# Kernel tuning notes

Measured on AMD Instinct MI355X. Metric: run time of the kernel, lower is better.

Reference implementation:

```python
import jax, jax.numpy as jnp
import numpy as np

B, N, M, H, W = 8, 8192, 4096, 128, 128


def setup_inputs() -> dict:
    key = jax.random.key(0)
    k1, k2, k3, k4 = jax.random.split(key, 4)
    xc_off_grid = jax.random.uniform(k1, (B, N, 2), dtype=jnp.float32)
    yc_off_grid = jax.random.normal(k2, (B, N), dtype=jnp.float32)
    # regular grid coords: meshgrid of two sorted 1-D axes, stacked on last dim
    xs = jnp.linspace(0.0, 1.0, H, dtype=jnp.float32)
    ys = jnp.linspace(0.0, 1.0, W, dtype=jnp.float32)
    gx, gy = jnp.meshgrid(xs, ys, indexing='ij')  # [H,W]
    xc_on_grid = jnp.broadcast_to(jnp.stack([gx, gy], -1), (B, H, W, 2))
    yc_on_grid = jax.random.normal(k3, (B, H, W), dtype=jnp.float32)
    # targets slightly outside [0,1] so interpn fill_value path is exercised
    xt = jax.random.uniform(k4, (B, M, 2), minval=-0.05, maxval=1.05, dtype=jnp.float32)
    mix_prop_logit = jnp.asarray(0.0, dtype=jnp.float32)
    return {"xc_off_grid": xc_off_grid, "yc_off_grid": yc_off_grid,
            "xc_on_grid": xc_on_grid, "yc_on_grid": yc_on_grid,
            "xt": xt, "mix_prop_logit": mix_prop_logit}


def _bilinear(xs, ys, vals, pts, fill):
    # interpn((xs, ys), vals, pts, bounds_error=False, fill_value=fill)
    x, y = pts[:, 0], pts[:, 1]
    ix = jnp.clip(jnp.searchsorted(xs, x, side='right') - 1, 0, xs.shape[0] - 2)
    iy = jnp.clip(jnp.searchsorted(ys, y, side='right') - 1, 0, ys.shape[0] - 2)
    wx = (x - xs[ix]) / (xs[ix + 1] - xs[ix])
    wy = (y - ys[iy]) / (ys[iy + 1] - ys[iy])
    v00 = vals[ix, iy]
    v01 = vals[ix, iy + 1]
    v10 = vals[ix + 1, iy]
    v11 = vals[ix + 1, iy + 1]
    v = ((1 - wx) * (1 - wy) * v00 + (1 - wx) * wy * v01
         + wx * (1 - wy) * v10 + wx * wy * v11)
    oob = (x < xs[0]) | (x > xs[-1]) | (y < ys[0]) | (y > ys[-1])
    return jnp.where(oob, fill, v)


def _per_batch(xc_off, yc_off, xc_on, yc_on, pts):
    # scattered interpolation: nearest-neighbor gather (stands in for
    # scipy griddata's Delaunay-linear; same irregular-access pattern)
    d2 = jnp.sum((pts[:, None, :] - xc_off[None, :, :]) ** 2, axis=-1)  # [M,N]
    yt_off = yc_off[jnp.argmin(d2, axis=1)]  # [M]
    # regular-grid bilinear, fill with grid mean outside bounds
    yt_on = _bilinear(xc_on[:, 0, 0], xc_on[0, :, 1], yc_on, pts, yc_on.mean())
    return yt_off, yt_on


def reference(xc_off_grid, yc_off_grid, xc_on_grid, yc_on_grid, xt, mix_prop_logit):
    yt_off, yt_on = jax.vmap(_per_batch)(xc_off_grid, yc_off_grid,
                                         xc_on_grid, yc_on_grid, xt)
    mix = jax.nn.sigmoid(mix_prop_logit)
    return mix * yt_off + (1 - mix) * yt_on  # [B, M]
```

## Files before the change

### kernel.cpp

```cpp
#include <hip/hip_runtime.h>
#include <math.h>
#include <float.h>

#define BB 8
#define NN 8192
#define MM 4096
#define HH 128
#define WW 128

#define G    32
#define GG   (G * G)
#define CELL (1.0f / G)

#define WS_COUNTS_OFF 256
#define WS_STARTS_OFF 33024
#define WS_CELLS_OFF  65824
#define WS_NEEDED     (WS_CELLS_OFF + (size_t)BB * NN * 16)

__device__ __forceinline__ int clampi(int v, int lo, int hi) {
    return v < lo ? lo : (v > hi ? hi : v);
}

__global__ __launch_bounds__(256)
void count_kernel(const float* __restrict__ xc_off,
                  int* __restrict__ counts) {
    const int idx = blockIdx.x * blockDim.x + threadIdx.x;
    const int b = idx >> 13;
    const float2 c = ((const float2*)xc_off)[idx];
    const int gx = clampi((int)(c.x * (float)G), 0, G - 1);
    const int gy = clampi((int)(c.y * (float)G), 0, G - 1);
    atomicAdd(&counts[b * GG + gx * G + gy], 1);
}

__global__ __launch_bounds__(1024)
void scan_mean_kernel(int* __restrict__ counts,
                      int* __restrict__ starts,
                      const float* __restrict__ yc_on,
                      float* __restrict__ means) {
    const int b = blockIdx.x, tid = threadIdx.x;
    __shared__ int   wsum[16];
    __shared__ float partial[4];

    const int orig = counts[b * GG + tid];
    int x = orig;
    const int lane = tid & 63, wid = tid >> 6;
    for (int off = 1; off < 64; off <<= 1) {
        int y = __shfl_up(x, off, 64);
        if (lane >= off) x += y;
    }
    if (lane == 63) wsum[wid] = x;
    __syncthreads();
    if (tid < 16) {
        int w = wsum[tid];
        for (int off = 1; off < 16; off <<= 1) {
            int y = __shfl_up(w, off, 16);
            if (tid >= off) w += y;
        }
        wsum[tid] = w;
    }
    __syncthreads();
    const int incl = x + (wid ? wsum[wid - 1] : 0);
    const int excl = incl - orig;
    starts[b * (GG + 1) + tid] = excl;
    if (tid == GG - 1) starts[b * (GG + 1) + GG] = incl;
    counts[b * GG + tid] = excl;

    float s = 0.f;
    if (tid < 256) {
        const float* p = yc_on + b * (HH * WW);
        for (int i = tid; i < HH * WW; i += 256) s += p[i];
        for (int off = 32; off > 0; off >>= 1) s += __shfl_down(s, off, 64);
    }
    if (tid < 256 && (tid & 63) == 0) partial[tid >> 6] = s;
    __syncthreads();
    if (tid == 0) {
        float t = 0.f;
        for (int i = 0; i < 4; ++i) t += partial[i];
        means[b] = t * (1.0f / (HH * WW));
    }
}

__global__ __launch_bounds__(256)
void scatter_kernel(const float* __restrict__ xc_off,
                    const float* __restrict__ yc_off,
                    int* __restrict__ cursors,
                    float4* __restrict__ cellData) {
    const int idx = blockIdx.x * blockDim.x + threadIdx.x;
    const int b = idx >> 13;
    const int n = idx & (NN - 1);
    const float2 c = ((const float2*)xc_off)[idx];
    const float v = yc_off[idx];
    const int gx = clampi((int)(c.x * (float)G), 0, G - 1);
    const int gy = clampi((int)(c.y * (float)G), 0, G - 1);
    const int pos = atomicAdd(&cursors[b * GG + gx * G + gy], 1);
    cellData[(size_t)b * NN + pos] = make_float4(c.x, c.y, v, __int_as_float(n));
}

__device__ __forceinline__ float epilogue(const float* __restrict__ yc_on,
                                          const float* __restrict__ means,
                                          const float* __restrict__ logit_p,
                                          int b, float px, float py, float bv) {
    const float* __restrict__ vals = yc_on + (size_t)b * HH * WW;
    const float x = px, y = py;
    int ix = clampi((int)floorf(x * 127.0f), 0, 126);
    int iy = clampi((int)floorf(y * 127.0f), 0, 126);
    const float x0 = (float)ix * (1.0f / 127.0f);
    const float x1 = (float)(ix + 1) * (1.0f / 127.0f);
    const float y0 = (float)iy * (1.0f / 127.0f);
    const float y1 = (float)(iy + 1) * (1.0f / 127.0f);
    const float wx = (x - x0) / (x1 - x0);
    const float wy = (y - y0) / (y1 - y0);
    const float v00 = vals[ix * WW + iy];
    const float v01 = vals[ix * WW + iy + 1];
    const float v10 = vals[(ix + 1) * WW + iy];
    const float v11 = vals[(ix + 1) * WW + iy + 1];
    float vi = (1.f - wx) * (1.f - wy) * v00
             + (1.f - wx) * wy         * v01
             + wx         * (1.f - wy) * v10
             + wx         * wy         * v11;
    const bool oob = (x < 0.f) || (x > 1.f) || (y < 0.f) || (y > 1.f);
    const float yon = oob ? means[b] : vi;
    const float l   = logit_p[0];
    const float mix = 1.f / (1.f + expf(-l));
    return mix * bv + (1.f - mix) * yon;
}

__global__ __launch_bounds__(256)
void query_kernel(const int* __restrict__ starts,
                  const float4* __restrict__ cellData,
                  const float* __restrict__ yc_on,
                  const float* __restrict__ xt,
                  const float* __restrict__ means,
                  const float* __restrict__ logit_p,
                  float* __restrict__ out)
{
    const int lane32 = threadIdx.x & 31;
    const int pid = blockIdx.x * 8 + (threadIdx.x >> 5);
    const int b = pid >> 12;
    const int m = pid & (MM - 1);

    const float2 pt = ((const float2*)xt)[pid];
    const float px = pt.x, py = pt.y;

    const int cx = clampi((int)(px * (float)G), 0, G - 1);
    const int cy = clampi((int)(py * (float)G), 0, G - 1);

    const int*    __restrict__ st = starts + b * (GG + 1);
    const float4* __restrict__ cd = cellData + (size_t)b * NN;

    float bd = FLT_MAX;
    float bv = 0.f;
    int   bi = 0x7fffffff;

    for (int r = 1; r <= G; ++r) {
        const int gx0 = clampi(cx - r, 0, G - 1);
        const int gx1 = clampi(cx + r, 0, G - 1);
        const int gy0 = clampi(cy - r, 0, G - 1);
        const int gy1 = clampi(cy + r, 0, G - 1);

        for (int gx = gx0; gx <= gx1; ++gx) {
            const int lo = st[gx * G + gy0];
            const int hi = st[gx * G + gy1 + 1];
            for (int j = lo + lane32; j < hi; j += 32) {
                const float4 c = cd[j];
                const float dx = px - c.x;
                const float dy = py - c.y;
                const float d2 = fmaf(dx, dx, dy * dy);
                const int   ci = __float_as_int(c.w);
                if (d2 < bd || (d2 == bd && ci < bi)) { bd = d2; bv = c.z; bi = ci; }
            }
        }

        for (int off = 1; off < 32; off <<= 1) {
            const float od = __shfl_xor(bd, off, 64);
            const float ov = __shfl_xor(bv, off, 64);
            const int   oi = __shfl_xor(bi, off, 64);
            if (od < bd || (od == bd && oi < bi)) { bd = od; bv = ov; bi = oi; }
        }

        const float rr = (float)r * CELL;
        if (rr * rr > bd) break;
    }

    if (lane32 == 0)
        out[(size_t)b * MM + m] = epilogue(yc_on, means, logit_p, b, px, py, bv);
}

#define WAVES 8
#define PTS 64
#define SLICE (NN / WAVES)

__global__ void mean_kernel(const float* __restrict__ yc_on,
                            float* __restrict__ means) {
    int b = blockIdx.x;
    const float* p = yc_on + b * (HH * WW);
    float s = 0.f;
    for (int i = threadIdx.x; i < HH * WW; i += blockDim.x) s += p[i];
    for (int off = 32; off > 0; off >>= 1) s += __shfl_down(s, off, 64);
    __shared__ float partial[4];
    int wave = threadIdx.x >> 6;
    if ((threadIdx.x & 63) == 0) partial[wave] = s;
    __syncthreads();
    if (threadIdx.x == 0) {
        float t = 0.f;
        int nw = blockDim.x >> 6;
        for (int i = 0; i < nw; ++i) t += partial[i];
        means[b] = t * (1.0f / (HH * WW));
    }
}

__global__ __launch_bounds__(WAVES * 64)
void nn_kernel(const float* __restrict__ xc_off,
               const float* __restrict__ yc_off,
               const float* __restrict__ yc_on,
               const float* __restrict__ xt,
               const float* __restrict__ means,
               const float* __restrict__ logit_p,
               float* __restrict__ out)
{
    const int blocksPerBatch = MM / PTS;
    const int b     = blockIdx.x / blocksPerBatch;
    const int pbase = (blockIdx.x % blocksPerBatch) * PTS;
    const int wave  = threadIdx.x >> 6;
    const int lane  = threadIdx.x & 63;
    const int m     = pbase + lane;

    const float2 pt = ((const float2*)xt)[b * MM + m];
    const float px = pt.x, py = pt.y;

    const float2* __restrict__ cxy = ((const float2*)xc_off) + (size_t)b * NN;
    const float*  __restrict__ cv  = yc_off + (size_t)b * NN;

    float best = 3.4e38f, bestv = 0.f;
    const int j0 = wave * SLICE;
    for (int t = 0; t < SLICE; t += 8) {
#pragma unroll
        for (int u = 0; u < 8; ++u) {
            const int j = j0 + t + u;
            const float2 c = cxy[j];
            const float  v = cv[j];
            const float dx = px - c.x;
            const float dy = py - c.y;
            const float d2 = fmaf(dx, dx, dy * dy);
            const bool lt = d2 < best;
            best  = lt ? d2 : best;
            bestv = lt ? v  : bestv;
        }
    }

    __shared__ float sd2[WAVES][PTS];
    __shared__ float sv [WAVES][PTS];
    sd2[wave][lane] = best;
    sv [wave][lane] = bestv;
    __syncthreads();

    if (threadIdx.x < PTS) {
        float bd = sd2[0][lane];
        float bv = sv [0][lane];
#pragma unroll
        for (int wv = 1; wv < WAVES; ++wv) {
            if (sd2[wv][lane] < bd) { bd = sd2[wv][lane]; bv = sv[wv][lane]; }
        }
        out[(size_t)b * MM + m] = epilogue(yc_on, means, logit_p, b, px, py, bv);
    }
}

extern "C" void kernel_launch(void* const* d_in, const int* in_sizes, int n_in,
                              void* d_out, int out_size, void* d_ws, size_t ws_size,
                              hipStream_t stream) {
    const float* xc_off = (const float*)d_in[0];
    const float* yc_off = (const float*)d_in[1];
    const float* yc_on  = (const float*)d_in[3];
    const float* xt     = (const float*)d_in[4];
    const float* logit  = (const float*)d_in[5];
    float* out = (float*)d_out;

    float* means = (float*)d_ws;

    if (ws_size >= WS_NEEDED) {
        int*    counts   = (int*)((char*)d_ws + WS_COUNTS_OFF);
        int*    starts   = (int*)((char*)d_ws + WS_STARTS_OFF);
        float4* cellData = (float4*)((char*)d_ws + WS_CELLS_OFF);

        hipMemsetAsync(counts, 0, (size_t)BB * GG * sizeof(int), stream);
        count_kernel<<<(BB * NN) / 256, 256, 0, stream>>>(xc_off, counts);
        scan_mean_kernel<<<BB, 1024, 0, stream>>>(counts, starts, yc_on, means);
        scatter_kernel<<<(BB * NN) / 256, 256, 0, stream>>>(
            xc_off, yc_off, counts, cellData);
        query_kernel<<<(BB * MM) / 8, 256, 0, stream>>>(
            starts, cellData, yc_on, xt, means, logit, out);
    } else {
        mean_kernel<<<BB, 256, 0, stream>>>(yc_on, means);
        nn_kernel<<<BB * (MM / PTS), WAVES * 64, 0, stream>>>(
            xc_off, yc_off, yc_on, xt, means, logit, out);
    }
}
```

Before: 105.9 us.

## Fuse counting, scan and scatter into one per-batch binning kernel with LDS atomics

Replaces the memset, global-atomic count kernel, scan kernel and global-atomic scatter kernel with a single kernel per batch that counts cell occupancy in shared memory, scans it, and scatters points into cell order using shared-memory atomics. This removes three launches plus a memset and the global atomic traffic. The cost is that binning now runs on only 8 workgroups, one per batch, so the preprocessing is much less parallel.

```diff
diff --git a/kernel.cpp b/kernel.cpp
--- a/kernel.cpp
+++ b/kernel.cpp
@@ -12,36 +12,45 @@
 #define GG   (G * G)
 #define CELL (1.0f / G)
 
-#define WS_COUNTS_OFF 256
-#define WS_STARTS_OFF 33024
-#define WS_CELLS_OFF  65824
+#define WS_STARTS_OFF 256
+#define WS_CELLS_OFF  33056
 #define WS_NEEDED     (WS_CELLS_OFF + (size_t)BB * NN * 16)
 
 __device__ __forceinline__ int clampi(int v, int lo, int hi) {
     return v < lo ? lo : (v > hi ? hi : v);
 }
 
-__global__ __launch_bounds__(256)
-void count_kernel(const float* __restrict__ xc_off,
-                  int* __restrict__ counts) {
-    const int idx = blockIdx.x * blockDim.x + threadIdx.x;
-    const int b = idx >> 13;
-    const float2 c = ((const float2*)xc_off)[idx];
-    const int gx = clampi((int)(c.x * (float)G), 0, G - 1);
-    const int gy = clampi((int)(c.y * (float)G), 0, G - 1);
-    atomicAdd(&counts[b * GG + gx * G + gy], 1);
-}
-
 __global__ __launch_bounds__(1024)
-void scan_mean_kernel(int* __restrict__ counts,
-                      int* __restrict__ starts,
-                      const float* __restrict__ yc_on,
-                      float* __restrict__ means) {
-    const int b = blockIdx.x, tid = threadIdx.x;
+void bin_mean_kernel(const float* __restrict__ xc_off,
+                     const float* __restrict__ yc_off,
+                     const float* __restrict__ yc_on,
+                     int* __restrict__ starts,
+                     float4* __restrict__ cellData,
+                     float* __restrict__ means)
+{
+    const int b   = blockIdx.x;
+    const int tid = threadIdx.x;
+    __shared__ int   cnt[GG];
     __shared__ int   wsum[16];
     __shared__ float partial[4];
-
-    const int orig = counts[b * GG + tid];
+    cnt[tid] = 0;
+    __syncthreads();
+
+    const float2* __restrict__ cxy = ((const float2*)xc_off) + (size_t)b * NN;
+    float2 pts[NN / 1024];
+    int    cells[NN / 1024];
+#pragma unroll
+    for (int k = 0; k < NN / 1024; ++k) {
+        float2 c = cxy[tid + k * 1024];
+        int gx = clampi((int)(c.x * (float)G), 0, G - 1);
+        int gy = clampi((int)(c.y * (float)G), 0, G - 1);
+        pts[k]   = c;
+        cells[k] = gx * G + gy;
+        atomicAdd(&cnt[cells[k]], 1);
+    }
+    __syncthreads();
+
+    const int orig = cnt[tid];
     int x = orig;
     const int lane = tid & 63, wid = tid >> 6;
     for (int off = 1; off < 64; off <<= 1) {
@@ -63,7 +72,19 @@
     const int excl = incl - orig;
     starts[b * (GG + 1) + tid] = excl;
     if (tid == GG - 1) starts[b * (GG + 1) + GG] = incl;
-    counts[b * GG + tid] = excl;
+    __syncthreads();
+    cnt[tid] = excl;
+    __syncthreads();
+
+    const float* __restrict__ cv = yc_off + (size_t)b * NN;
+#pragma unroll
+    for (int k = 0; k < NN / 1024; ++k) {
+        const int i = tid + k * 1024;
+        const float v = cv[i];
+        const int pos = atomicAdd(&cnt[cells[k]], 1);
+        cellData[(size_t)b * NN + pos] =
+            make_float4(pts[k].x, pts[k].y, v, __int_as_float(i));
+    }
 
     float s = 0.f;
     if (tid < 256) {
@@ -78,22 +99,6 @@
         for (int i = 0; i < 4; ++i) t += partial[i];
         means[b] = t * (1.0f / (HH * WW));
     }
-}
-
-__global__ __launch_bounds__(256)
-void scatter_kernel(const float* __restrict__ xc_off,
-                    const float* __restrict__ yc_off,
-                    int* __restrict__ cursors,
-                    float4* __restrict__ cellData) {
-    const int idx = blockIdx.x * blockDim.x + threadIdx.x;
-    const int b = idx >> 13;
-    const int n = idx & (NN - 1);
-    const float2 c = ((const float2*)xc_off)[idx];
-    const float v = yc_off[idx];
-    const int gx = clampi((int)(c.x * (float)G), 0, G - 1);
-    const int gy = clampi((int)(c.y * (float)G), 0, G - 1);
-    const int pos = atomicAdd(&cursors[b * GG + gx * G + gy], 1);
-    cellData[(size_t)b * NN + pos] = make_float4(c.x, c.y, v, __int_as_float(n));
 }
 
 __device__ __forceinline__ float epilogue(const float* __restrict__ yc_on,
@@ -278,15 +283,11 @@
     float* means = (float*)d_ws;
 
     if (ws_size >= WS_NEEDED) {
-        int*    counts   = (int*)((char*)d_ws + WS_COUNTS_OFF);
         int*    starts   = (int*)((char*)d_ws + WS_STARTS_OFF);
         float4* cellData = (float4*)((char*)d_ws + WS_CELLS_OFF);
 
-        hipMemsetAsync(counts, 0, (size_t)BB * GG * sizeof(int), stream);
-        count_kernel<<<(BB * NN) / 256, 256, 0, stream>>>(xc_off, counts);
-        scan_mean_kernel<<<BB, 1024, 0, stream>>>(counts, starts, yc_on, means);
-        scatter_kernel<<<(BB * NN) / 256, 256, 0, stream>>>(
-            xc_off, yc_off, counts, cellData);
+        bin_mean_kernel<<<BB, 1024, 0, stream>>>(
+            xc_off, yc_off, yc_on, starts, cellData, means);
         query_kernel<<<(BB * MM) / 8, 256, 0, stream>>>(
             starts, cellData, yc_on, xt, means, logit, out);
     } else {
```

Result: no change. 104.9 us (-0.9%).
